# Performance work log

Measured on AMD Instinct MI355X. Metric: run time of the kernel, lower is better.

## Reference

```python
import jax, jax.numpy as jnp
import numpy as np

NH, HD = 4, 16          # num_heads, head_dim (proj_dim = 64)
SCALE = HD ** -0.5
EPS = 1e-5
G = 16                  # GroupNorm groups = min(16, channels)


def _conv1x1(W, b, x):
    # 1x1 conv == channel-mixing matmul: W (out,in), x (B,in,H,W)
    return jnp.einsum('pc,bchw->bphw', W, x) + b[None, :, None, None]


def _attend(Wq, bq, Wk, bk, Wv, bv, Wo, bo, query, context):
    B, C, H, Wd = query.shape
    N = H * Wd
    q = _conv1x1(Wq, bq, query).astype(jnp.float32).reshape(B, NH, HD, N)
    k = _conv1x1(Wk, bk, context).astype(jnp.float32).reshape(B, NH, HD, N)
    v = _conv1x1(Wv, bv, context).astype(jnp.float32).reshape(B, NH, HD, N)
    attn = jax.nn.softmax(jnp.einsum('bhdn,bhdm->bhnm', q, k) * SCALE, axis=-1)
    out = jnp.einsum('bhdm,bhnm->bhdn', v, attn).reshape(B, NH * HD, H, Wd)
    return _conv1x1(Wo, bo, out)


def _gn(x, gamma, beta):
    B, C, H, W = x.shape
    xr = x.reshape(B, G, C // G, H, W)
    m = xr.mean(axis=(2, 3, 4), keepdims=True)
    v = xr.var(axis=(2, 3, 4), keepdims=True)
    xn = ((xr - m) * jax.lax.rsqrt(v + EPS)).reshape(B, C, H, W)
    return xn * gamma[None, :, None, None] + beta[None, :, None, None]


def setup_inputs() -> dict:
    key = jax.random.key(0)
    C, P, Bn, H, W = 256, 64, 2, 64, 64
    ks = iter(jax.random.split(key, 64))
    d = {}
    for m in ['a', 'b', 'c']:
        d[f'feat_{m}'] = jax.random.normal(next(ks), (Bn, C, H, W), jnp.float32)
    for m in ['a', 'b', 'c']:
        d[f'Wq_{m}'] = 0.02 * jax.random.normal(next(ks), (P, C), jnp.float32)
        d[f'bq_{m}'] = jnp.zeros((P,), jnp.float32)
        d[f'Wk_{m}'] = 0.02 * jax.random.normal(next(ks), (P, 2 * C), jnp.float32)
        d[f'bk_{m}'] = jnp.zeros((P,), jnp.float32)
        d[f'Wv_{m}'] = 0.02 * jax.random.normal(next(ks), (P, 2 * C), jnp.float32)
        d[f'bv_{m}'] = jnp.zeros((P,), jnp.float32)
        d[f'Wo_{m}'] = 0.02 * jax.random.normal(next(ks), (C, P), jnp.float32)
        d[f'bo_{m}'] = jnp.zeros((C,), jnp.float32)
        d[f'g_{m}'] = jnp.ones((C,), jnp.float32)
        d[f'be_{m}'] = jnp.zeros((C,), jnp.float32)
    return d


def reference(feat_a, feat_b, feat_c,
              Wq_a, bq_a, Wk_a, bk_a, Wv_a, bv_a, Wo_a, bo_a, g_a, be_a,
              Wq_b, bq_b, Wk_b, bk_b, Wv_b, bv_b, Wo_b, bo_b, g_b, be_b,
              Wq_c, bq_c, Wk_c, bk_c, Wv_c, bv_c, Wo_c, bo_c, g_c, be_c):
    bc = jnp.concatenate([feat_b, feat_c], axis=1)
    a_out = _gn(feat_a + _attend(Wq_a, bq_a, Wk_a, bk_a, Wv_a, bv_a, Wo_a, bo_a, feat_a, bc), g_a, be_a)
    ac = jnp.concatenate([feat_a, feat_c], axis=1)
    b_out = _gn(feat_b + _attend(Wq_b, bq_b, Wk_b, bk_b, Wv_b, bv_b, Wo_b, bo_b, feat_b, ac), g_b, be_b)
    ab = jnp.concatenate([feat_a, feat_b], axis=1)
    c_out = _gn(feat_c + _attend(Wq_c, bq_c, Wk_c, bk_c, Wv_c, bv_c, Wo_c, bo_c, feat_c, ab), g_c, be_c)
    return (a_out, b_out, c_out)
```

## Files before the change

### kernel.cpp

```cpp
#include <hip/hip_runtime.h>

#define B_ 2
#define C_ 256
#define P_ 64
#define N_ 4096
#define EPS_ 1e-5f
#define QSCALE_ 0.3606737602222409f

typedef _Float16 half4 __attribute__((ext_vector_type(4)));
typedef _Float16 half8 __attribute__((ext_vector_type(8)));
typedef float f32x4 __attribute__((ext_vector_type(4)));

static __device__ __forceinline__ float fexp2(float x) {
  return __builtin_bit_cast(float, (int)fmaf(x, 8388608.0f, 1064872512.0f));
}

struct TP {
  const float* feat[3];
  const float* Wq[3]; const float* bq[3];
  const float* Wk[3]; const float* bk[3];
  const float* Wv[3]; const float* bv[3];
  const float* Wo[3]; const float* bo[3];
  const float* gm[3]; const float* bt[3];
  _Float16* q16;
  _Float16* k16;
  _Float16* v16;
  _Float16* ao0;
  _Float16* ao1;
  float* L;
  float* stats;
  float* out;
  int ctx0[3]; int ctx1[3];
};

#define PST_ 264
#define VTS_ 88

__global__ __launch_bounds__(256) void proj_fused_kernel(TP P) {
  __shared__ _Float16 bs[64 * PST_];
  const int m = blockIdx.z, b = blockIdx.y;
  const int tid = threadIdx.x;
  const int w = tid >> 6, g = (tid >> 4) & 3, t = tid & 15;
  const bool is_q = blockIdx.x >= 64;
  const int n0 = (is_q ? blockIdx.x - 64 : (int)blockIdx.x) * 64;
  const int sn = tid & 63, scb = (tid >> 6) * 16;

  if (is_q) {
    const float* __restrict__ in = P.feat[m] + (size_t)b * C_ * N_ + n0 + sn;
#pragma unroll
    for (int cc = 0; cc < 4; ++cc) {
      const int c0 = cc * 64 + scb;
      float f[16];
#pragma unroll
      for (int i = 0; i < 16; ++i) f[i] = in[(size_t)(c0 + i) * N_];
      half8 h0, h1;
#pragma unroll
      for (int j = 0; j < 8; ++j) { h0[j] = (_Float16)f[j]; h1[j] = (_Float16)f[8 + j]; }
      *(half8*)(bs + sn * PST_ + c0) = h0;
      *(half8*)(bs + sn * PST_ + c0 + 8) = h1;
    }
    __syncthreads();
    f32x4 a[4] = {{0.f,0.f,0.f,0.f},{0.f,0.f,0.f,0.f},{0.f,0.f,0.f,0.f},{0.f,0.f,0.f,0.f}};
    const float* __restrict__ Wq = P.Wq[m] + (w * 16 + t) * 256;
#pragma unroll
    for (int ks = 0; ks < 8; ++ks) {
      const float4 wa = *(const float4*)(Wq + ks * 32 + g * 8);
      const float4 wb = *(const float4*)(Wq + ks * 32 + g * 8 + 4);
      half8 af;
      af[0] = (_Float16)wa.x; af[1] = (_Float16)wa.y;
      af[2] = (_Float16)wa.z; af[3] = (_Float16)wa.w;
      af[4] = (_Float16)wb.x; af[5] = (_Float16)wb.y;
      af[6] = (_Float16)wb.z; af[7] = (_Float16)wb.w;
#pragma unroll
      for (int i = 0; i < 4; ++i) {
        const half8 bf = *(const half8*)(bs + (i * 16 + t) * PST_ + ks * 32 + g * 8);
        a[i] = __builtin_amdgcn_mfma_f32_16x16x32_f16(af, bf, a[i], 0, 0, 0);
      }
    }
    float bq[4];
#pragma unroll
    for (int r = 0; r < 4; ++r) bq[r] = P.bq[m][w * 16 + g * 4 + r];
    _Float16* qo = P.q16 + ((size_t)(m * 2 + b) * N_) * 64 + w * 16 + g * 4;
#pragma unroll
    for (int i = 0; i < 4; ++i) {
      half4 hq;
#pragma unroll
      for (int r = 0; r < 4; ++r) hq[r] = (_Float16)((a[i][r] + bq[r]) * QSCALE_);
      *(half4*)(qo + (size_t)(n0 + i * 16 + t) * 64) = hq;
    }
  } else {
    f32x4 ka[4] = {{0.f,0.f,0.f,0.f},{0.f,0.f,0.f,0.f},{0.f,0.f,0.f,0.f},{0.f,0.f,0.f,0.f}};
    f32x4 va[4] = {{0.f,0.f,0.f,0.f},{0.f,0.f,0.f,0.f},{0.f,0.f,0.f,0.f},{0.f,0.f,0.f,0.f}};
    const int srcs[2] = {P.ctx0[m], P.ctx1[m]};
    for (int src = 0; src < 2; ++src) {
      const float* __restrict__ in =
          P.feat[srcs[src]] + (size_t)b * C_ * N_ + n0 + sn;
      if (src) __syncthreads();
#pragma unroll
      for (int cc = 0; cc < 4; ++cc) {
        const int c0 = cc * 64 + scb;
        float f[16];
#pragma unroll
        for (int i = 0; i < 16; ++i) f[i] = in[(size_t)(c0 + i) * N_];
        half8 h0, h1;
#pragma unroll
        for (int j = 0; j < 8; ++j) { h0[j] = (_Float16)f[j]; h1[j] = (_Float16)f[8 + j]; }
        *(half8*)(bs + sn * PST_ + c0) = h0;
        *(half8*)(bs + sn * PST_ + c0 + 8) = h1;
      }
      __syncthreads();
      const float* __restrict__ Wk = P.Wk[m] + (w * 16 + t) * 512 + src * 256;
      const float* __restrict__ Wv = P.Wv[m] + (w * 16 + t) * 512 + src * 256;
#pragma unroll
      for (int ks = 0; ks < 8; ++ks) {
        const float4 k0 = *(const float4*)(Wk + ks * 32 + g * 8);
        const float4 k1 = *(const float4*)(Wk + ks * 32 + g * 8 + 4);
        const float4 v0 = *(const float4*)(Wv + ks * 32 + g * 8);
        const float4 v1 = *(const float4*)(Wv + ks * 32 + g * 8 + 4);
        half8 ak, av;
        ak[0] = (_Float16)k0.x; ak[1] = (_Float16)k0.y;
        ak[2] = (_Float16)k0.z; ak[3] = (_Float16)k0.w;
        ak[4] = (_Float16)k1.x; ak[5] = (_Float16)k1.y;
        ak[6] = (_Float16)k1.z; ak[7] = (_Float16)k1.w;
        av[0] = (_Float16)v0.x; av[1] = (_Float16)v0.y;
        av[2] = (_Float16)v0.z; av[3] = (_Float16)v0.w;
        av[4] = (_Float16)v1.x; av[5] = (_Float16)v1.y;
        av[6] = (_Float16)v1.z; av[7] = (_Float16)v1.w;
#pragma unroll
        for (int i = 0; i < 4; ++i) {
          const half8 bf = *(const half8*)(bs + (i * 16 + t) * PST_ + ks * 32 + g * 8);
          ka[i] = __builtin_amdgcn_mfma_f32_16x16x32_f16(ak, bf, ka[i], 0, 0, 0);
          va[i] = __builtin_amdgcn_mfma_f32_16x16x32_f16(av, bf, va[i], 0, 0, 0);
        }
      }
    }
    float bk[4], bv[4];
#pragma unroll
    for (int r = 0; r < 4; ++r) {
      bk[r] = P.bk[m][w * 16 + g * 4 + r];
      bv[r] = P.bv[m][w * 16 + g * 4 + r];
    }
    _Float16* ko = P.k16 + ((size_t)(m * 8 + b * 4 + w) * N_) * 16 + g * 4;
#pragma unroll
    for (int i = 0; i < 4; ++i) {
      half4 hk;
#pragma unroll
      for (int r = 0; r < 4; ++r) hk[r] = (_Float16)(ka[i][r] + bk[r]);
      *(half4*)(ko + (size_t)(n0 + i * 16 + t) * 16) = hk;
    }
    __syncthreads();
#pragma unroll
    for (int i = 0; i < 4; ++i)
#pragma unroll
      for (int r = 0; r < 4; ++r)
        bs[(w * 16 + g * 4 + r) * VTS_ + i * 16 + t] = (_Float16)(va[i][r] + bv[r]);
    __syncthreads();
#pragma unroll
    for (int pass = 0; pass < 2; ++pass) {
      const int row = pass * 32 + (tid >> 3);
      const int hh = row >> 4, dd = row & 15, nb = (tid & 7) * 8;
      const half8 hv = *(const half8*)(bs + row * VTS_ + nb);
      *(half8*)(P.v16 + ((size_t)(m * 8 + b * 4 + hh) * 16 + dd) * N_ + n0 + nb) = hv;
    }
  }
}

#define KST_ 24

__global__ __launch_bounds__(512) void attn_kernel(TP P) {
  const int m = blockIdx.z, bh = blockIdx.y;
  const int tid = threadIdx.x;
  if (m == 0 && bh == 0 && blockIdx.x == 0 && tid < 192) P.stats[tid] = 0.f;
  const int kvh = blockIdx.x & 1, qb = blockIdx.x >> 1;
  const int kvbase = kvh * 2048;
  const int w = tid >> 6, g = (tid >> 4) & 3, t = tid & 15;
  const _Float16* __restrict__ kh = P.k16 + ((size_t)(m * 8 + bh) * N_) * 16;
  const _Float16* __restrict__ vh = P.v16 + ((size_t)(m * 8 + bh) * 16) * N_;
  const int b = bh >> 2, h = bh & 3;
  const _Float16* __restrict__ qh =
      P.q16 + ((size_t)(m * 2 + b) * N_) * 64 + h * 16 + g * 4;

  const int q0 = qb * 128 + w * 16;
  const half4 qf = *(const half4*)(qh + (size_t)(q0 + t) * 64);

  __shared__ _Float16 ks[256 * KST_];
  __shared__ _Float16 vs[16 * 256];

  const int kr = tid >> 1, kc8 = tid & 1;
  const int vr = tid >> 5, vc = tid & 31;
  const _Float16* kgp = kh + (size_t)(kvbase + kr) * 16 + kc8 * 8;
  const _Float16* vgp = vh + (size_t)vr * N_ + kvbase + vc * 8;
  _Float16* ksp = ks + kr * KST_ + kc8 * 8;
  _Float16* vsp = vs + vr * 256 + ((vc ^ vr) << 3);

  half8 kpre = *(const half8*)kgp;
  half8 vpre = *(const half8*)vgp;

  f32x4 lacc = {0.f, 0.f, 0.f, 0.f};
  f32x4 O0 = {0.f,0.f,0.f,0.f}, O1 = {0.f,0.f,0.f,0.f};

  for (int c0 = 0; c0 < 2048; c0 += 256) {
    *(half8*)ksp = kpre;
    *(half8*)vsp = vpre;
    __syncthreads();
    const int nxt = (c0 + 256 < 2048) ? c0 + 256 : 0;
    kpre = *(const half8*)(kgp + (size_t)nxt * 16);
    vpre = *(const half8*)(vgp + nxt);
#pragma unroll
    for (int hc = 0; hc < 4; ++hc) {
      f32x4 s[4];
#pragma unroll
      for (int i = 0; i < 4; ++i) {
        const int sub = hc * 4 + i;
        const half4 kf = *(const half4*)(ks + (sub * 16 + t) * KST_ +
                                         (g >> 1) * 8 + (g & 1) * 4);
        const f32x4 z = {0.f, 0.f, 0.f, 0.f};
        s[i] = __builtin_amdgcn_mfma_f32_16x16x16f16(kf, qf, z, 0, 0, 0);
      }
      half4 pf[4];
#pragma unroll
      for (int i = 0; i < 4; ++i) {
        const float p0 = fexp2(s[i][0]), p1 = fexp2(s[i][1]);
        const float p2 = fexp2(s[i][2]), p3 = fexp2(s[i][3]);
        lacc[0] += p0; lacc[1] += p1; lacc[2] += p2; lacc[3] += p3;
        pf[i][0] = (_Float16)p0; pf[i][1] = (_Float16)p1;
        pf[i][2] = (_Float16)p2; pf[i][3] = (_Float16)p3;
      }
#pragma unroll
      for (int i = 0; i < 4; ++i) {
        const int c = (hc * 4 + i) * 2 + (g >> 1);
        const half4 vf = *(const half4*)(vs + t * 256 + ((c ^ t) << 3) + (g & 1) * 4);
        if (i & 1) O1 = __builtin_amdgcn_mfma_f32_16x16x16f16(vf, pf[i], O1, 0, 0, 0);
        else       O0 = __builtin_amdgcn_mfma_f32_16x16x16f16(vf, pf[i], O0, 0, 0, 0);
      }
    }
    __syncthreads();
  }
  float l = lacc[0] + lacc[1] + lacc[2] + lacc[3];
  l += __shfl_xor(l, 16);
  l += __shfl_xor(l, 32);
  _Float16* aop = (kvh ? P.ao1 : P.ao0) +
                  ((size_t)(m * 2 + b) * N_ + q0 + t) * 64 + h * 16 + g * 4;
  half4 hv;
#pragma unroll
  for (int r = 0; r < 4; ++r) hv[r] = (_Float16)(O0[r] + O1[r]);
  *(half4*)aop = hv;
  if (g == 0 && (tid & 48) == 0)
    P.L[((size_t)(kvh * 3 + m) * 8 + bh) * N_ + q0 + t] = l;
}

#define BS_ 72

__global__ __launch_bounds__(256) void wo_resid_kernel(TP P) {
  __shared__ _Float16 as[64 * BS_];
  const int m = blockIdx.z;
  const int b = blockIdx.y >> 2, cblk = blockIdx.y & 3;
  const int n0 = blockIdx.x * 64;
  const int tid = threadIdx.x;
  const int w = tid >> 6, g = (tid >> 4) & 3, t = tid & 15;
  const int c0 = cblk * 64 + w * 16;
  const size_t aob = ((size_t)(m * 2 + b) * N_) * 64;
  const _Float16* __restrict__ a0p = P.ao0 + aob;
  const _Float16* __restrict__ a1p = P.ao1 + aob;
  const int ar = tid >> 2, ac = (tid & 3) * 16;
  {
    const size_t off = (size_t)(n0 + ar) * 64 + ac;
    half8 s0 = *(const half8*)(a0p + off);
    half8 s1 = *(const half8*)(a0p + off + 8);
    const half8 u0 = *(const half8*)(a1p + off);
    const half8 u1 = *(const half8*)(a1p + off + 8);
#pragma unroll
    for (int r = 0; r < 8; ++r) { s0[r] += u0[r]; s1[r] += u1[r]; }
    *(half8*)(as + ar * BS_ + ac) = s0;
    *(half8*)(as + ar * BS_ + ac + 8) = s1;
  }
  __syncthreads();
  const float* __restrict__ L0 = P.L + ((size_t)m * 8 + b * 4) * N_;
  const float* __restrict__ L1 = P.L + ((size_t)(3 + m) * 8 + b * 4) * N_;
  f32x4 acc[4] = {{0.f,0.f,0.f,0.f},{0.f,0.f,0.f,0.f},{0.f,0.f,0.f,0.f},{0.f,0.f,0.f,0.f}};
  const float* __restrict__ Wo = P.Wo[m] + (c0 + t) * 64;
#pragma unroll
  for (int kst = 0; kst < 2; ++kst) {
    const float4 w0 = *(const float4*)(Wo + kst * 32 + g * 8);
    const float4 w1 = *(const float4*)(Wo + kst * 32 + g * 8 + 4);
    half8 a;
    a[0] = (_Float16)w0.x; a[1] = (_Float16)w0.y;
    a[2] = (_Float16)w0.z; a[3] = (_Float16)w0.w;
    a[4] = (_Float16)w1.x; a[5] = (_Float16)w1.y;
    a[6] = (_Float16)w1.z; a[7] = (_Float16)w1.w;
    const int head = kst * 2 + (g >> 1);
#pragma unroll
    for (int i = 0; i < 4; ++i) {
      const int n = n0 + i * 16 + t;
      half8 bf = *(const half8*)(as + (i * 16 + t) * BS_ + kst * 32 + g * 8);
      const float ls = L0[(size_t)head * N_ + n] + L1[(size_t)head * N_ + n];
      const _Float16 hs = (_Float16)(1.0f / ls);
#pragma unroll
      for (int r = 0; r < 8; ++r) bf[r] *= hs;
      acc[i] = __builtin_amdgcn_mfma_f32_16x16x32_f16(a, bf, acc[i], 0, 0, 0);
    }
  }
  const float* __restrict__ X = P.feat[m] + (size_t)b * C_ * N_;
  float* outb = P.out + (size_t)m * B_ * C_ * N_ + (size_t)b * C_ * N_;
  float s = 0.f, s2 = 0.f;
#pragma unroll
  for (int i = 0; i < 4; ++i) {
    const int n = n0 + i * 16 + t;
#pragma unroll
    for (int r = 0; r < 4; ++r) {
      const int c = c0 + g * 4 + r;
      const float val = acc[i][r] + X[(size_t)c * N_ + n] + P.bo[m][c];
      outb[(size_t)c * N_ + n] = val;
      s += val;
      s2 += val * val;
    }
  }
#pragma unroll
  for (int off = 1; off < 64; off <<= 1) {
    s += __shfl_xor(s, off);
    s2 += __shfl_xor(s2, off);
  }
  if ((tid & 63) == 0) {
    const int group = cblk * 4 + w;
    float* st = P.stats + ((size_t)(m * 2 + b) * 16 + group) * 2;
    atomicAdd(st, s);
    atomicAdd(st + 1, s2);
  }
}

__global__ __launch_bounds__(256) void gn_final_kernel(TP P) {
  const size_t base = ((size_t)blockIdx.x * 256 + threadIdx.x) * 4;
#pragma unroll
  for (int it = 0; it < 4; ++it) {
    const size_t idx = base + (size_t)it * 1572864;
    const int m = (int)(idx >> 21);
    const int rem = (int)(idx & ((1u << 21) - 1));
    const int b = rem >> 20;
    const int c = (rem >> 12) & 255;
    const float* st = P.stats + ((size_t)(m * 2 + b) * 16 + (c >> 4)) * 2;
    const float mean = st[0] * (1.f / 65536.f);
    const float var = st[1] * (1.f / 65536.f) - mean * mean;
    const float rstd = rsqrtf(var + EPS_);
    const float ga = P.gm[m][c] * rstd, be = P.bt[m][c];
    float4 x = *(float4*)(P.out + idx);
    x.x = (x.x - mean) * ga + be;
    x.y = (x.y - mean) * ga + be;
    x.z = (x.z - mean) * ga + be;
    x.w = (x.w - mean) * ga + be;
    *(float4*)(P.out + idx) = x;
  }
}

extern "C" void kernel_launch(void* const* d_in, const int* in_sizes, int n_in,
                              void* d_out, int out_size, void* d_ws, size_t ws_size,
                              hipStream_t stream) {
  TP P;
  for (int m = 0; m < 3; ++m) {
    P.feat[m] = (const float*)d_in[m];
    const int base = 3 + m * 10;
    P.Wq[m] = (const float*)d_in[base + 0];
    P.bq[m] = (const float*)d_in[base + 1];
    P.Wk[m] = (const float*)d_in[base + 2];
    P.bk[m] = (const float*)d_in[base + 3];
    P.Wv[m] = (const float*)d_in[base + 4];
    P.bv[m] = (const float*)d_in[base + 5];
    P.Wo[m] = (const float*)d_in[base + 6];
    P.bo[m] = (const float*)d_in[base + 7];
    P.gm[m] = (const float*)d_in[base + 8];
    P.bt[m] = (const float*)d_in[base + 9];
  }
  _Float16* ws = (_Float16*)d_ws;
  P.q16 = ws;
  P.k16 = ws + 1572864;
  P.v16 = ws + 3145728;
  P.ao0 = ws + 4718592;
  P.ao1 = ws + 6291456;
  P.L = (float*)(ws + 7864320);
  P.stats = (float*)(ws + 7864320) + 196608;
  P.out = (float*)d_out;
  P.ctx0[0] = 1; P.ctx1[0] = 2;
  P.ctx0[1] = 0; P.ctx1[1] = 2;
  P.ctx0[2] = 0; P.ctx1[2] = 1;

  proj_fused_kernel<<<dim3(128, 2, 3), dim3(256), 0, stream>>>(P);
  attn_kernel<<<dim3(64, 8, 3), dim3(512), 0, stream>>>(P);
  wo_resid_kernel<<<dim3(64, 8, 3), dim3(256), 0, stream>>>(P);
  gn_final_kernel<<<dim3(1536), dim3(256), 0, stream>>>(P);
}
```

Measured before the change: 271.8 us.

## Switch attention to 32x32x16 MFMA with packed fp16 exp and fused row-sum

Reworks the attention inner loop to use 32x32x16 MFMA tiles, with 256 queries per block, so the grid halves. The exponential is now built by scaling q by 1024·log2e, biasing the score accumulator, then converting to u32 and packing to u16. The packed integers are fp16 bit patterns of exp2. The P fragments are rearranged with v_permlane32_swap and the row sums come from an extra all-ones row in V, so the separate lacc accumulation and shuffles go away. This cuts VALU work per score and the number of MFMA issues, but the bit-trick exp is cruder and negative or overflowing exponents now depend on clamping during the u32/u16 conversion.

Measured after the change: 252.4 us. 1.08x faster.

```diff
diff --git a/kernel.cpp b/kernel.cpp
--- a/kernel.cpp
+++ b/kernel.cpp
@@ -5,14 +5,22 @@
 #define P_ 64
 #define N_ 4096
 #define EPS_ 1e-5f
-#define QSCALE_ 0.3606737602222409f
+#define QSCALE1024_ 369.32993046757467f
 
 typedef _Float16 half4 __attribute__((ext_vector_type(4)));
 typedef _Float16 half8 __attribute__((ext_vector_type(8)));
 typedef float f32x4 __attribute__((ext_vector_type(4)));
-
-static __device__ __forceinline__ float fexp2(float x) {
-  return __builtin_bit_cast(float, (int)fmaf(x, 8388608.0f, 1064872512.0f));
+typedef float f32x16 __attribute__((ext_vector_type(16)));
+typedef unsigned int uint4v __attribute__((ext_vector_type(4)));
+
+static __device__ __forceinline__ unsigned int pkexp2(float t0, float t1) {
+  unsigned int pk, tmp;
+  asm("v_cvt_u32_f32 %0, %2\n\t"
+      "v_cvt_u32_f32 %1, %3\n\t"
+      "v_cvt_pk_u16_u32 %0, %0, %1"
+      : "=&v"(pk), "=&v"(tmp)
+      : "v"(t0), "v"(t1));
+  return pk;
 }
 
 struct TP {
@@ -85,7 +93,7 @@
     for (int i = 0; i < 4; ++i) {
       half4 hq;
 #pragma unroll
-      for (int r = 0; r < 4; ++r) hq[r] = (_Float16)((a[i][r] + bq[r]) * QSCALE_);
+      for (int r = 0; r < 4; ++r) hq[r] = (_Float16)((a[i][r] + bq[r]) * QSCALE1024_);
       *(half4*)(qo + (size_t)(n0 + i * 16 + t) * 64) = hq;
     }
   } else {
@@ -166,6 +174,7 @@
 }
 
 #define KST_ 24
+#define VST_ 264
 
 __global__ __launch_bounds__(512) void attn_kernel(TP P) {
   const int m = blockIdx.z, bh = blockIdx.y;
@@ -173,31 +182,40 @@
   if (m == 0 && bh == 0 && blockIdx.x == 0 && tid < 192) P.stats[tid] = 0.f;
   const int kvh = blockIdx.x & 1, qb = blockIdx.x >> 1;
   const int kvbase = kvh * 2048;
-  const int w = tid >> 6, g = (tid >> 4) & 3, t = tid & 15;
+  const int w = tid >> 6;
+  const int lane = tid & 63;
+  const int n = lane & 31;
+  const int hh = lane >> 5;
+  const int b = bh >> 2, h = bh & 3;
   const _Float16* __restrict__ kh = P.k16 + ((size_t)(m * 8 + bh) * N_) * 16;
   const _Float16* __restrict__ vh = P.v16 + ((size_t)(m * 8 + bh) * 16) * N_;
-  const int b = bh >> 2, h = bh & 3;
-  const _Float16* __restrict__ qh =
-      P.q16 + ((size_t)(m * 2 + b) * N_) * 64 + h * 16 + g * 4;
-
-  const int q0 = qb * 128 + w * 16;
-  const half4 qf = *(const half4*)(qh + (size_t)(q0 + t) * 64);
+  const int q0 = qb * 256 + w * 32;
+  const half8 qf = *(const half8*)(P.q16 +
+      ((size_t)(m * 2 + b) * N_ + q0 + n) * 64 + h * 16 + hh * 8);
 
   __shared__ _Float16 ks[256 * KST_];
-  __shared__ _Float16 vs[16 * 256];
+  __shared__ _Float16 vs[32 * VST_];
+
+  if (tid < 32) {
+    half8 o8;
+#pragma unroll
+    for (int j = 0; j < 8; ++j) o8[j] = (_Float16)1.0f;
+    *(half8*)(vs + 16 * VST_ + tid * 8) = o8;
+  }
 
   const int kr = tid >> 1, kc8 = tid & 1;
   const int vr = tid >> 5, vc = tid & 31;
   const _Float16* kgp = kh + (size_t)(kvbase + kr) * 16 + kc8 * 8;
   const _Float16* vgp = vh + (size_t)vr * N_ + kvbase + vc * 8;
   _Float16* ksp = ks + kr * KST_ + kc8 * 8;
-  _Float16* vsp = vs + vr * 256 + ((vc ^ vr) << 3);
+  _Float16* vsp = vs + vr * VST_ + vc * 8;
 
   half8 kpre = *(const half8*)kgp;
   half8 vpre = *(const half8*)vgp;
 
-  f32x4 lacc = {0.f, 0.f, 0.f, 0.f};
-  f32x4 O0 = {0.f,0.f,0.f,0.f}, O1 = {0.f,0.f,0.f,0.f};
+  f32x16 Z, Oe, Oo;
+#pragma unroll
+  for (int r = 0; r < 16; ++r) { Z[r] = 15360.5f; Oe[r] = 0.f; Oo[r] = 0.f; }
 
   for (int c0 = 0; c0 < 2048; c0 += 256) {
     *(half8*)ksp = kpre;
@@ -207,46 +225,49 @@
     kpre = *(const half8*)(kgp + (size_t)nxt * 16);
     vpre = *(const half8*)(vgp + nxt);
 #pragma unroll
-    for (int hc = 0; hc < 4; ++hc) {
-      f32x4 s[4];
-#pragma unroll
-      for (int i = 0; i < 4; ++i) {
-        const int sub = hc * 4 + i;
-        const half4 kf = *(const half4*)(ks + (sub * 16 + t) * KST_ +
-                                         (g >> 1) * 8 + (g & 1) * 4);
-        const f32x4 z = {0.f, 0.f, 0.f, 0.f};
-        s[i] = __builtin_amdgcn_mfma_f32_16x16x16f16(kf, qf, z, 0, 0, 0);
-      }
-      half4 pf[4];
-#pragma unroll
-      for (int i = 0; i < 4; ++i) {
-        const float p0 = fexp2(s[i][0]), p1 = fexp2(s[i][1]);
-        const float p2 = fexp2(s[i][2]), p3 = fexp2(s[i][3]);
-        lacc[0] += p0; lacc[1] += p1; lacc[2] += p2; lacc[3] += p3;
-        pf[i][0] = (_Float16)p0; pf[i][1] = (_Float16)p1;
-        pf[i][2] = (_Float16)p2; pf[i][3] = (_Float16)p3;
-      }
-#pragma unroll
-      for (int i = 0; i < 4; ++i) {
-        const int c = (hc * 4 + i) * 2 + (g >> 1);
-        const half4 vf = *(const half4*)(vs + t * 256 + ((c ^ t) << 3) + (g & 1) * 4);
-        if (i & 1) O1 = __builtin_amdgcn_mfma_f32_16x16x16f16(vf, pf[i], O1, 0, 0, 0);
-        else       O0 = __builtin_amdgcn_mfma_f32_16x16x16f16(vf, pf[i], O0, 0, 0, 0);
-      }
+    for (int sub = 0; sub < 8; ++sub) {
+      const half8 kf = *(const half8*)(ks + (sub * 32 + n) * KST_ + hh * 8);
+      const f32x16 s = __builtin_amdgcn_mfma_f32_32x32x16_f16(kf, qf, Z, 0, 0, 0);
+      unsigned int p0 = pkexp2(s[0], s[1]);
+      unsigned int p1 = pkexp2(s[2], s[3]);
+      unsigned int p2 = pkexp2(s[4], s[5]);
+      unsigned int p3 = pkexp2(s[6], s[7]);
+      unsigned int p4 = pkexp2(s[8], s[9]);
+      unsigned int p5 = pkexp2(s[10], s[11]);
+      unsigned int p6 = pkexp2(s[12], s[13]);
+      unsigned int p7 = pkexp2(s[14], s[15]);
+      asm("v_permlane32_swap_b32 %0, %1" : "+v"(p2), "+v"(p0));
+      asm("v_permlane32_swap_b32 %0, %1" : "+v"(p3), "+v"(p1));
+      asm("v_permlane32_swap_b32 %0, %1" : "+v"(p6), "+v"(p4));
+      asm("v_permlane32_swap_b32 %0, %1" : "+v"(p7), "+v"(p5));
+      const uint4v ua = {p0, p1, p2, p3};
+      const uint4v ub = {p4, p5, p6, p7};
+      const half8 ve = *(const half8*)(vs + n * VST_ + sub * 32 + hh * 8);
+      const half8 vo = *(const half8*)(vs + n * VST_ + sub * 32 + 16 + hh * 8);
+      Oe = __builtin_amdgcn_mfma_f32_32x32x16_f16(
+          __builtin_bit_cast(half8, ua), ve, Oe, 0, 0, 0);
+      Oo = __builtin_amdgcn_mfma_f32_32x32x16_f16(
+          __builtin_bit_cast(half8, ub), vo, Oo, 0, 0, 0);
     }
     __syncthreads();
   }
-  float l = lacc[0] + lacc[1] + lacc[2] + lacc[3];
-  l += __shfl_xor(l, 16);
-  l += __shfl_xor(l, 32);
-  _Float16* aop = (kvh ? P.ao1 : P.ao0) +
-                  ((size_t)(m * 2 + b) * N_ + q0 + t) * 64 + h * 16 + g * 4;
-  half4 hv;
-#pragma unroll
-  for (int r = 0; r < 4; ++r) hv[r] = (_Float16)(O0[r] + O1[r]);
-  *(half4*)aop = hv;
-  if (g == 0 && (tid & 48) == 0)
-    P.L[((size_t)(kvh * 3 + m) * 8 + bh) * N_ + q0 + t] = l;
+
+  if (n < 16) {
+    _Float16* aop = (kvh ? P.ao1 : P.ao0) +
+                    ((size_t)(m * 2 + b) * N_ + q0) * 64 + h * 16 + n;
+#pragma unroll
+    for (int r = 0; r < 16; ++r) {
+      const int qrow = (r & 3) + 8 * (r >> 2) + 4 * hh;
+      aop[(size_t)qrow * 64] = (_Float16)(Oe[r] + Oo[r]);
+    }
+  } else if (n == 16) {
+    float* Lp = P.L + ((size_t)(kvh * 3 + m) * 8 + bh) * N_ + q0;
+#pragma unroll
+    for (int r = 0; r < 16; ++r) {
+      const int qrow = (r & 3) + 8 * (r >> 2) + 4 * hh;
+      Lp[qrow] = Oe[r] + Oo[r];
+    }
+  }
 }
 
 #define BS_ 72
@@ -291,9 +312,9 @@
     const int head = kst * 2 + (g >> 1);
 #pragma unroll
     for (int i = 0; i < 4; ++i) {
-      const int n = n0 + i * 16 + t;
+      const int nn = n0 + i * 16 + t;
       half8 bf = *(const half8*)(as + (i * 16 + t) * BS_ + kst * 32 + g * 8);
-      const float ls = L0[(size_t)head * N_ + n] + L1[(size_t)head * N_ + n];
+      const float ls = L0[(size_t)head * N_ + nn] + L1[(size_t)head * N_ + nn];
       const _Float16 hs = (_Float16)(1.0f / ls);
 #pragma unroll
       for (int r = 0; r < 8; ++r) bf[r] *= hs;
@@ -305,12 +326,12 @@
   float s = 0.f, s2 = 0.f;
 #pragma unroll
   for (int i = 0; i < 4; ++i) {
-    const int n = n0 + i * 16 + t;
+    const int nn = n0 + i * 16 + t;
 #pragma unroll
     for (int r = 0; r < 4; ++r) {
       const int c = c0 + g * 4 + r;
-      const float val = acc[i][r] + X[(size_t)c * N_ + n] + P.bo[m][c];
-      outb[(size_t)c * N_ + n] = val;
+      const float val = acc[i][r] + X[(size_t)c * N_ + nn] + P.bo[m][c];
+      outb[(size_t)c * N_ + nn] = val;
       s += val;
       s2 += val * val;
     }
@@ -383,7 +404,7 @@
   P.ctx0[2] = 0; P.ctx1[2] = 1;
 
   proj_fused_kernel<<<dim3(128, 2, 3), dim3(256), 0, stream>>>(P);
-  attn_kernel<<<dim3(64, 8, 3), dim3(512), 0, stream>>>(P);
+  attn_kernel<<<dim3(32, 8, 3), dim3(512), 0, stream>>>(P);
   wo_resid_kernel<<<dim3(64, 8, 3), dim3(256), 0, stream>>>(P);
   gn_final_kernel<<<dim3(1536), dim3(256), 0, stream>>>(P);
 }
```
